# Optimization experiments

Measured on AMD Instinct MI355X. Metric: run time of the kernel, lower is better.

The kernel has to match this reference:

```python
import jax, jax.numpy as jnp
import numpy as np

N_HEADS = 16
D_HEAD = 64
D_MODEL = 1024
WINDOW = 256
B, T = 4, 2048


def rotate_half(x):
    x1, x2 = jnp.split(x, 2, axis=-1)
    return jnp.concatenate([-x2, x1], axis=-1)


def apply_rope(x, cos, sin):
    return x * cos + rotate_half(x) * sin


def setup_inputs() -> dict:
    key = jax.random.key(0)
    ks = jax.random.split(key, 5)
    x = jax.random.normal(ks[0], (B, T, D_MODEL), dtype=jnp.float32)
    cos = jax.random.normal(ks[1], (1, T, 1, D_HEAD), dtype=jnp.float32)
    sin = jax.random.normal(ks[2], (1, T, 1, D_HEAD), dtype=jnp.float32)
    qkv_w = jax.random.normal(ks[3], (3 * D_MODEL, D_MODEL), dtype=jnp.float32) * (D_MODEL ** -0.5)
    out_w = jax.random.normal(ks[4], (D_MODEL, D_MODEL), dtype=jnp.float32) * (D_MODEL ** -0.5)
    return {"x": x, "cos": cos, "sin": sin, "qkv_w": qkv_w, "out_w": out_w}


def reference(x, cos, sin, qkv_w, out_w):
    Bc, Tc, C = x.shape
    # QKV projection (bias-free Linear: y = x @ W^T)
    qkv = jnp.einsum('btc,fc->btf', x, qkv_w)
    q, k, v = jnp.split(qkv, 3, axis=-1)
    # [B, H, T, d]
    def to_heads(t):
        return t.reshape(Bc, Tc, N_HEADS, D_HEAD).transpose(0, 2, 1, 3)
    q, k, v = to_heads(q), to_heads(k), to_heads(v)
    # RoPE: cos/sin [1, T, 1, d] -> [1, 1, T, d] broadcasting over heads
    cos_t = cos[:, :Tc].transpose(0, 2, 1, 3)
    sin_t = sin[:, :Tc].transpose(0, 2, 1, 3)
    q = apply_rope(q, cos_t, sin_t)
    k = apply_rope(k, cos_t, sin_t)
    # banded causal mask: allow j <= i and j >= i - (window-1)
    i = jnp.arange(Tc)[:, None]
    j = jnp.arange(Tc)[None, :]
    allowed = (j <= i) & (j >= i - (WINDOW - 1))  # [T, T]
    scale = 1.0 / jnp.sqrt(jnp.asarray(D_HEAD, dtype=q.dtype))
    scores = jnp.einsum('bhqd,bhkd->bhqk', q, k) * scale
    scores = jnp.where(allowed[None, None], scores, jnp.finfo(scores.dtype).min)
    attn = jax.nn.softmax(scores, axis=-1)
    out = jnp.einsum('bhqk,bhkd->bhqd', attn, v)
    out = out.transpose(0, 2, 1, 3).reshape(Bc, Tc, C)
    return jnp.einsum('btc,oc->bto', out, out_w)
```

## Files before the change

kernel.cpp:

```cpp
#include <hip/hip_runtime.h>

typedef __bf16 bf16_t;
typedef __bf16 bf16x8 __attribute__((ext_vector_type(8)));
typedef __bf16 bf16x4 __attribute__((ext_vector_type(4)));
typedef float f32x4 __attribute__((ext_vector_type(4)));

#define GLOAD_LDS16(gptr, lptr)                                                              \
  __builtin_amdgcn_global_load_lds((const __attribute__((address_space(1))) void*)(gptr),    \
                                   (__attribute__((address_space(3))) void*)(lptr), 16, 0, 0)

__device__ __forceinline__ f32x4 f32x4_zero() {
  f32x4 v; v[0] = 0.f; v[1] = 0.f; v[2] = 0.f; v[3] = 0.f; return v;
}

__global__ void cast3_kernel(const float* __restrict__ a, const float* __restrict__ b,
                             const float* __restrict__ c, bf16_t* __restrict__ oa,
                             bf16_t* __restrict__ ob, bf16_t* __restrict__ oc) {
  int i = blockIdx.x * blockDim.x + threadIdx.x;
  const float* src; bf16_t* dst; int j;
  if (i < 2097152) { src = a; dst = oa; j = i; }
  else if (i < 2883584) { src = b; dst = ob; j = i - 2097152; }
  else { src = c; dst = oc; j = i - 2883584; }
  float4 v = ((const float4*)src)[j];
  bf16x4 o;
  o[0] = (bf16_t)v.x; o[1] = (bf16_t)v.y; o[2] = (bf16_t)v.z; o[3] = (bf16_t)v.w;
  ((bf16x4*)dst)[j] = o;
}

#define GT_AELE 16384
#define GT_BELE 8192
#define GT_TILE (GT_AELE + GT_BELE)

__device__ __forceinline__ void gt_stage(const bf16_t* __restrict__ A,
                                         const bf16_t* __restrict__ B, bf16_t* buf,
                                         int bm, int bn, int t, int K, int tid) {
#pragma unroll
  for (int i = 0; i < 4; i++) {
    int gi = tid + i * 512;
    int row = gi >> 3, g = gi & 7;
    const bf16_t* src = A + (size_t)(bm * 256 + row) * K + t * 64 + ((g ^ (row & 7)) << 3);
    GLOAD_LDS16(src, buf + gi * 8);
  }
#pragma unroll
  for (int i = 0; i < 2; i++) {
    int gi = tid + i * 512;
    int row = gi >> 3, g = gi & 7;
    const bf16_t* src = B + (size_t)(bn * 128 + row) * K + t * 64 + ((g ^ (row & 7)) << 3);
    GLOAD_LDS16(src, buf + GT_AELE + gi * 8);
  }
}

template <int MODE>
__global__ __launch_bounds__(512, 1) void gemm_bt_kernel(
    const bf16_t* __restrict__ A, const bf16_t* __restrict__ B, float* __restrict__ C,
    bf16_t* __restrict__ oq, bf16_t* __restrict__ ok_, bf16_t* __restrict__ ov,
    const float* __restrict__ cosp, const float* __restrict__ sinp,
    int M, int N, int K) {
  __shared__ bf16_t lds[3 * GT_TILE];

  const int tid = threadIdx.x;
  const int lane = tid & 63;
  const int wid = tid >> 6;
  const int wr = wid >> 1;
  const int wc = wid & 1;
  const int l16 = lane & 15;
  const int qd = lane >> 4;
  const int bm = blockIdx.x, bn = blockIdx.y;

  f32x4 acc[4][4];
#pragma unroll
  for (int m = 0; m < 4; m++)
#pragma unroll
    for (int n = 0; n < 4; n++) acc[m][n] = f32x4_zero();

  const int NT = K >> 6;

  gt_stage(A, B, lds, bm, bn, 0, K, tid);
  gt_stage(A, B, lds + GT_TILE, bm, bn, 1, K, tid);
  asm volatile("s_waitcnt vmcnt(6)" ::: "memory");
  __builtin_amdgcn_s_barrier();
  __builtin_amdgcn_sched_barrier(0);

  int s = 0;
  for (int j = 0; j < NT; ++j) {
    if (j + 2 < NT) {
      int s2 = s + 2; if (s2 >= 3) s2 -= 3;
      gt_stage(A, B, lds + s2 * GT_TILE, bm, bn, j + 2, K, tid);
    }

    const bf16_t* bufc = lds + s * GT_TILE;
    bf16x8 af[4][2], bf[4][2];
#pragma unroll
    for (int m = 0; m < 4; m++)
#pragma unroll
      for (int kk = 0; kk < 2; kk++) {
        int row = wr * 64 + m * 16 + l16;
        af[m][kk] = *(const bf16x8*)&bufc[row * 64 + (((kk * 4 + qd) ^ (row & 7)) << 3)];
      }
#pragma unroll
    for (int n = 0; n < 4; n++)
#pragma unroll
      for (int kk = 0; kk < 2; kk++) {
        int row = wc * 64 + n * 16 + l16;
        bf[n][kk] = *(const bf16x8*)&bufc[GT_AELE + row * 64 + (((kk * 4 + qd) ^ (row & 7)) << 3)];
      }

    __builtin_amdgcn_s_setprio(1);
#pragma unroll
    for (int m = 0; m < 4; m++)
#pragma unroll
      for (int n = 0; n < 4; n++)
#pragma unroll
        for (int kk = 0; kk < 2; kk++)
          acc[m][n] = __builtin_amdgcn_mfma_f32_16x16x32_bf16(af[m][kk], bf[n][kk], acc[m][n], 0, 0, 0);
    __builtin_amdgcn_s_setprio(0);

    if (j + 2 < NT) {
      asm volatile("s_waitcnt vmcnt(6)" ::: "memory");
    } else {
      asm volatile("s_waitcnt vmcnt(0)" ::: "memory");
    }
    __builtin_amdgcn_s_barrier();
    __builtin_amdgcn_sched_barrier(0);
    s = (s == 2) ? 0 : s + 1;
  }

  if (MODE == 0) {
#pragma unroll
    for (int m = 0; m < 4; m++)
#pragma unroll
      for (int n = 0; n < 4; n++)
#pragma unroll
        for (int r = 0; r < 4; r++) {
          int row = bm * 256 + wr * 64 + m * 16 + qd * 4 + r;
          int col = bn * 128 + wc * 64 + n * 16 + l16;
          C[(size_t)row * N + col] = acc[m][n][r];
        }
  } else {
    const int colbase = bn * 128 + wc * 64;
    const int part = colbase >> 10;
    const int h = (colbase & 1023) >> 6;
    if (part == 2) {
      bf16_t* lw = lds + wid * 4096;
#pragma unroll
      for (int m = 0; m < 4; m++)
#pragma unroll
        for (int n = 0; n < 4; n++) {
          int d = n * 16 + l16;
          int gr = (m * 2 + (qd >> 1)) ^ (d & 7);
          bf16x4 w;
          w[0] = (bf16_t)acc[m][n][0];
          w[1] = (bf16_t)acc[m][n][1];
          w[2] = (bf16_t)acc[m][n][2];
          w[3] = (bf16_t)acc[m][n][3];
          *(bf16x4*)&lw[d * 64 + gr * 8 + (qd & 1) * 4] = w;
        }
      asm volatile("s_waitcnt lgkmcnt(0)" ::: "memory");
      __builtin_amdgcn_sched_barrier(0);
      const int rowbase = bm * 256 + wr * 64;
      const int bb = rowbase >> 11, tb = rowbase & 2047;
      bf16_t* vbase = ov + ((size_t)(bb * 16 + h) * 64) * 2048 + tb;
#pragma unroll
      for (int it = 0; it < 8; it++) {
        int d = it * 8 + (lane >> 3);
        int g = lane & 7;
        *(bf16x8*)&vbase[(size_t)d * 2048 + g * 8] =
            *(const bf16x8*)&lw[d * 64 + ((g ^ (d & 7)) << 3)];
      }
    } else {
      bf16_t* dst = (part == 0) ? oq : ok_;
      const float qsc = (part == 0) ? 0.18033688011112042f : 1.0f;
#pragma unroll
      for (int m = 0; m < 4; m++)
#pragma unroll
        for (int r = 0; r < 4; r++) {
          int row = bm * 256 + wr * 64 + m * 16 + qd * 4 + r;
          int b = row >> 11, t = row & 2047;
          size_t basei = (((size_t)(b * 16 + h)) * 2048 + t) * 64;
#pragma unroll
          for (int nb = 0; nb < 2; nb++) {
            int d = nb * 16 + l16;
            float xl = acc[m][nb][r];
            float xh = acc[m][nb + 2][r];
            float cl = cosp[t * 64 + d], ch = cosp[t * 64 + d + 32];
            float sl = sinp[t * 64 + d], sh = sinp[t * 64 + d + 32];
            dst[basei + d]      = (bf16_t)((xl * cl - xh * sl) * qsc);
            dst[basei + d + 32] = (bf16_t)((xh * ch + xl * sh) * qsc);
          }
        }
    }
  }
}

__global__ __launch_bounds__(256) void attn_kernel(
    const bf16_t* __restrict__ qh, const bf16_t* __restrict__ kh,
    const bf16_t* __restrict__ vt, bf16_t* __restrict__ ao) {
  __shared__ bf16_t qs[64 * 64];
  __shared__ bf16_t ks[64 * 64];
  __shared__ bf16_t vts[64 * 64];
  __shared__ bf16_t ps[4][16 * 64];

  const int tid = threadIdx.x;
  const int lane = tid & 63;
  const int wid = tid >> 6;
  const int l16 = lane & 15;
  const int qd = lane >> 4;

  const int bh = blockIdx.x;
  const int i0 = blockIdx.y * 64;
  const int b = bh >> 4, h = bh & 15;

  auto swz4 = [](int f) { int r = f >> 3; return r * 8 + ((f & 7) ^ (r & 7)); };

  {
    const uint4* src = (const uint4*)(qh + ((size_t)bh * 2048 + i0) * 64);
    uint4* dst = (uint4*)qs;
    dst[swz4(tid)] = src[tid];
    dst[swz4(tid + 256)] = src[tid + 256];
  }

  bf16x8 bones;
#pragma unroll
  for (int e = 0; e < 8; e++) bones[e] = (bf16_t)1.0f;

  float l_i[4] = {0.f, 0.f, 0.f, 0.f};
  f32x4 oacc[4];
#pragma unroll
  for (int nb = 0; nb < 4; nb++) oacc[nb] = f32x4_zero();

  const int c1 = i0 >> 6;
  const int c0 = (c1 >= 4) ? (c1 - 4) : 0;

  for (int c = c0; c <= c1; c++) {
    const int j0 = c * 64;
    __syncthreads();
    {
      const uint4* ksrc = (const uint4*)(kh + ((size_t)bh * 2048 + j0) * 64);
      uint4* kdst = (uint4*)ks;
      uint4* vdst = (uint4*)vts;
      kdst[swz4(tid)] = ksrc[tid];
      kdst[swz4(tid + 256)] = ksrc[tid + 256];
      {
        int f = tid;
        vdst[swz4(f)] = *(const uint4*)(vt + (size_t)(bh * 64 + (f >> 3)) * 2048 + j0 + (f & 7) * 8);
        f = tid + 256;
        vdst[swz4(f)] = *(const uint4*)(vt + (size_t)(bh * 64 + (f >> 3)) * 2048 + j0 + (f & 7) * 8);
      }
    }
    __syncthreads();

    f32x4 sacc[4];
#pragma unroll
    for (int nb = 0; nb < 4; nb++) sacc[nb] = f32x4_zero();
#pragma unroll
    for (int kk = 0; kk < 2; kk++) {
      bf16x8 afr = *(const bf16x8*)&qs[(wid * 16 + l16) * 64 + (((kk * 4 + qd) ^ (l16 & 7)) * 8)];
#pragma unroll
      for (int nb = 0; nb < 4; nb++) {
        bf16x8 bfr = *(const bf16x8*)&ks[(nb * 16 + l16) * 64 + (((kk * 4 + qd) ^ (l16 & 7)) * 8)];
        sacc[nb] = __builtin_amdgcn_mfma_f32_16x16x32_bf16(afr, bfr, sacc[nb], 0, 0, 0);
      }
    }

#pragma unroll
    for (int r = 0; r < 4; r++) {
      const int i = i0 + wid * 16 + qd * 4 + r;
      const int prow = qd * 4 + r;
#pragma unroll
      for (int nb = 0; nb < 4; nb++) {
        const int j = j0 + nb * 16 + l16;
        bool valid = (j <= i) && (j + 256 > i);
        float p = valid ? exp2f(sacc[nb][r]) : 0.f;
        ps[wid][prow * 64 + (((nb * 2 + (l16 >> 3)) ^ (prow & 7)) * 8) + (l16 & 7)] = (bf16_t)p;
      }
    }

    asm volatile("s_waitcnt lgkmcnt(0)" ::: "memory");
    __builtin_amdgcn_sched_barrier(0);

    f32x4 lacc = f32x4_zero();
#pragma unroll
    for (int kk = 0; kk < 2; kk++) {
      bf16x8 afr = *(const bf16x8*)&ps[wid][l16 * 64 + (((kk * 4 + qd) ^ (l16 & 7)) * 8)];
      lacc = __builtin_amdgcn_mfma_f32_16x16x32_bf16(afr, bones, lacc, 0, 0, 0);
#pragma unroll
      for (int nb = 0; nb < 4; nb++) {
        bf16x8 bfr = *(const bf16x8*)&vts[(nb * 16 + l16) * 64 + (((kk * 4 + qd) ^ (l16 & 7)) * 8)];
        oacc[nb] = __builtin_amdgcn_mfma_f32_16x16x32_bf16(afr, bfr, oacc[nb], 0, 0, 0);
      }
    }
#pragma unroll
    for (int r = 0; r < 4; r++) l_i[r] += lacc[r];
  }

#pragma unroll
  for (int nb = 0; nb < 4; nb++) {
#pragma unroll
    for (int r = 0; r < 4; r++) {
      int t = i0 + wid * 16 + qd * 4 + r;
      ao[((size_t)(b * 2048 + t)) * 1024 + h * 64 + nb * 16 + l16] =
          (bf16_t)(oacc[nb][r] / l_i[r]);
    }
  }
}

extern "C" void kernel_launch(void* const* d_in, const int* in_sizes, int n_in,
                              void* d_out, int out_size, void* d_ws, size_t ws_size,
                              hipStream_t stream) {
  const float* x    = (const float*)d_in[0];
  const float* cosp = (const float*)d_in[1];
  const float* sinp = (const float*)d_in[2];
  const float* qkvw = (const float*)d_in[3];
  const float* outw = (const float*)d_in[4];
  float* out = (float*)d_out;

  char* ws = (char*)d_ws;
  bf16_t* xb  = (bf16_t*)(ws + 0);
  bf16_t* qwb = (bf16_t*)(ws + 16777216);
  bf16_t* owb = (bf16_t*)(ws + 23068672);
  bf16_t* qhp = (bf16_t*)(ws + 25165824);
  bf16_t* khp = (bf16_t*)(ws + 41943040);
  bf16_t* vtp = (bf16_t*)(ws + 58720256);
  bf16_t* aop = (bf16_t*)(ws + 75497472);

  cast3_kernel<<<12288, 256, 0, stream>>>(x, qkvw, outw, xb, qwb, owb);

  gemm_bt_kernel<1><<<dim3(32, 24), 512, 0, stream>>>(xb, qwb, nullptr, qhp, khp, vtp,
                                                      cosp, sinp, 8192, 3072, 1024);
  attn_kernel<<<dim3(64, 32), 256, 0, stream>>>(qhp, khp, vtp, aop);
  gemm_bt_kernel<0><<<dim3(32, 8), 512, 0, stream>>>(aop, owb, out, nullptr, nullptr, nullptr,
                                                     nullptr, nullptr, 8192, 1024, 1024);
}
```

Measured before the change: 214.2 us.

## Process four query tiles per attention block to reuse K/V tiles

Each attention block now covers 256 query rows as four 64-row tiles held in shared memory, instead of a single 64-row tile. It walks the K/V tiles of the combined band once and applies each loaded tile to every query tile whose window includes it. This cuts redundant global K/V loads, since each tile was previously fetched by up to five blocks. In exchange the grid shrinks fourfold, shared-memory and accumulator register use grow, and the per-block loop becomes longer and more serial. The K/V buffers are indexed by iteration parity, but both barriers remain, so loads do not actually overlap with compute.

```diff
diff --git a/kernel.cpp b/kernel.cpp
--- a/kernel.cpp
+++ b/kernel.cpp
@@ -195,9 +195,9 @@
 __global__ __launch_bounds__(256) void attn_kernel(
     const bf16_t* __restrict__ qh, const bf16_t* __restrict__ kh,
     const bf16_t* __restrict__ vt, bf16_t* __restrict__ ao) {
-  __shared__ bf16_t qs[64 * 64];
-  __shared__ bf16_t ks[64 * 64];
-  __shared__ bf16_t vts[64 * 64];
+  __shared__ bf16_t qs[4][64 * 64];
+  __shared__ bf16_t ks[2][64 * 64];
+  __shared__ bf16_t vts[2][64 * 64];
   __shared__ bf16_t ps[4][16 * 64];
 
   const int tid = threadIdx.x;
@@ -207,101 +207,116 @@
   const int qd = lane >> 4;
 
   const int bh = blockIdx.x;
-  const int i0 = blockIdx.y * 64;
+  const int chunk = blockIdx.y;
   const int b = bh >> 4, h = bh & 15;
 
   auto swz4 = [](int f) { int r = f >> 3; return r * 8 + ((f & 7) ^ (r & 7)); };
 
   {
-    const uint4* src = (const uint4*)(qh + ((size_t)bh * 2048 + i0) * 64);
-    uint4* dst = (uint4*)qs;
-    dst[swz4(tid)] = src[tid];
-    dst[swz4(tid + 256)] = src[tid + 256];
+    const uint4* src = (const uint4*)(qh + ((size_t)bh * 2048 + chunk * 256) * 64);
+#pragma unroll
+    for (int qt = 0; qt < 4; qt++) {
+      uint4* dst = (uint4*)qs[qt];
+      dst[swz4(tid)] = src[qt * 512 + tid];
+      dst[swz4(tid + 256)] = src[qt * 512 + tid + 256];
+    }
   }
 
   bf16x8 bones;
 #pragma unroll
   for (int e = 0; e < 8; e++) bones[e] = (bf16_t)1.0f;
 
-  float l_i[4] = {0.f, 0.f, 0.f, 0.f};
-  f32x4 oacc[4];
-#pragma unroll
-  for (int nb = 0; nb < 4; nb++) oacc[nb] = f32x4_zero();
-
-  const int c1 = i0 >> 6;
-  const int c0 = (c1 >= 4) ? (c1 - 4) : 0;
+  f32x4 oacc[4][4];
+  float l_i[4][4];
+#pragma unroll
+  for (int qt = 0; qt < 4; qt++)
+#pragma unroll
+    for (int nb = 0; nb < 4; nb++) {
+      oacc[qt][nb] = f32x4_zero();
+      l_i[qt][nb] = 0.f;
+    }
+
+  const int cbase = chunk * 4;
+  const int c0 = (cbase >= 4) ? cbase - 4 : 0;
+  const int c1 = cbase + 3;
 
   for (int c = c0; c <= c1; c++) {
-    const int j0 = c * 64;
+    const int p = c & 1;
     __syncthreads();
     {
-      const uint4* ksrc = (const uint4*)(kh + ((size_t)bh * 2048 + j0) * 64);
-      uint4* kdst = (uint4*)ks;
-      uint4* vdst = (uint4*)vts;
+      const uint4* ksrc = (const uint4*)(kh + ((size_t)bh * 2048 + c * 64) * 64);
+      uint4* kdst = (uint4*)ks[p];
+      uint4* vdst = (uint4*)vts[p];
       kdst[swz4(tid)] = ksrc[tid];
       kdst[swz4(tid + 256)] = ksrc[tid + 256];
-      {
-        int f = tid;
-        vdst[swz4(f)] = *(const uint4*)(vt + (size_t)(bh * 64 + (f >> 3)) * 2048 + j0 + (f & 7) * 8);
-        f = tid + 256;
-        vdst[swz4(f)] = *(const uint4*)(vt + (size_t)(bh * 64 + (f >> 3)) * 2048 + j0 + (f & 7) * 8);
-      }
+      int f = tid;
+      vdst[swz4(f)] = *(const uint4*)(vt + (size_t)(bh * 64 + (f >> 3)) * 2048 + c * 64 + (f & 7) * 8);
+      f = tid + 256;
+      vdst[swz4(f)] = *(const uint4*)(vt + (size_t)(bh * 64 + (f >> 3)) * 2048 + c * 64 + (f & 7) * 8);
     }
     __syncthreads();
 
-    f32x4 sacc[4];
-#pragma unroll
-    for (int nb = 0; nb < 4; nb++) sacc[nb] = f32x4_zero();
-#pragma unroll
-    for (int kk = 0; kk < 2; kk++) {
-      bf16x8 afr = *(const bf16x8*)&qs[(wid * 16 + l16) * 64 + (((kk * 4 + qd) ^ (l16 & 7)) * 8)];
-#pragma unroll
-      for (int nb = 0; nb < 4; nb++) {
-        bf16x8 bfr = *(const bf16x8*)&ks[(nb * 16 + l16) * 64 + (((kk * 4 + qd) ^ (l16 & 7)) * 8)];
-        sacc[nb] = __builtin_amdgcn_mfma_f32_16x16x32_bf16(afr, bfr, sacc[nb], 0, 0, 0);
-      }
-    }
-
-#pragma unroll
-    for (int r = 0; r < 4; r++) {
-      const int i = i0 + wid * 16 + qd * 4 + r;
-      const int prow = qd * 4 + r;
-#pragma unroll
-      for (int nb = 0; nb < 4; nb++) {
-        const int j = j0 + nb * 16 + l16;
-        bool valid = (j <= i) && (j + 256 > i);
-        float p = valid ? exp2f(sacc[nb][r]) : 0.f;
-        ps[wid][prow * 64 + (((nb * 2 + (l16 >> 3)) ^ (prow & 7)) * 8) + (l16 & 7)] = (bf16_t)p;
-      }
-    }
-
-    asm volatile("s_waitcnt lgkmcnt(0)" ::: "memory");
-    __builtin_amdgcn_sched_barrier(0);
-
-    f32x4 lacc = f32x4_zero();
-#pragma unroll
-    for (int kk = 0; kk < 2; kk++) {
-      bf16x8 afr = *(const bf16x8*)&ps[wid][l16 * 64 + (((kk * 4 + qd) ^ (l16 & 7)) * 8)];
-      lacc = __builtin_amdgcn_mfma_f32_16x16x32_bf16(afr, bones, lacc, 0, 0, 0);
-#pragma unroll
-      for (int nb = 0; nb < 4; nb++) {
-        bf16x8 bfr = *(const bf16x8*)&vts[(nb * 16 + l16) * 64 + (((kk * 4 + qd) ^ (l16 & 7)) * 8)];
-        oacc[nb] = __builtin_amdgcn_mfma_f32_16x16x32_bf16(afr, bfr, oacc[nb], 0, 0, 0);
-      }
-    }
-#pragma unroll
-    for (int r = 0; r < 4; r++) l_i[r] += lacc[r];
-  }
-
-#pragma unroll
-  for (int nb = 0; nb < 4; nb++) {
-#pragma unroll
-    for (int r = 0; r < 4; r++) {
-      int t = i0 + wid * 16 + qd * 4 + r;
-      ao[((size_t)(b * 2048 + t)) * 1024 + h * 64 + nb * 16 + l16] =
-          (bf16_t)(oacc[nb][r] / l_i[r]);
-    }
-  }
+    const int lc = c - cbase;
+#pragma unroll
+    for (int qt = 0; qt < 4; qt++) {
+      if (qt < lc || qt > lc + 4) continue;
+      const int i0q = chunk * 256 + qt * 64;
+
+      f32x4 sacc[4];
+#pragma unroll
+      for (int nb = 0; nb < 4; nb++) sacc[nb] = f32x4_zero();
+#pragma unroll
+      for (int kk = 0; kk < 2; kk++) {
+        bf16x8 afr = *(const bf16x8*)&qs[qt][(wid * 16 + l16) * 64 + (((kk * 4 + qd) ^ (l16 & 7)) * 8)];
+#pragma unroll
+        for (int nb = 0; nb < 4; nb++) {
+          bf16x8 bfr = *(const bf16x8*)&ks[p][(nb * 16 + l16) * 64 + (((kk * 4 + qd) ^ (l16 & 7)) * 8)];
+          sacc[nb] = __builtin_amdgcn_mfma_f32_16x16x32_bf16(afr, bfr, sacc[nb], 0, 0, 0);
+        }
+      }
+
+#pragma unroll
+      for (int r = 0; r < 4; r++) {
+        const int i = i0q + wid * 16 + qd * 4 + r;
+        const int prow = qd * 4 + r;
+#pragma unroll
+        for (int nb = 0; nb < 4; nb++) {
+          const int j = c * 64 + nb * 16 + l16;
+          bool valid = (j <= i) && (j + 256 > i);
+          float pv = valid ? exp2f(sacc[nb][r]) : 0.f;
+          ps[wid][prow * 64 + (((nb * 2 + (l16 >> 3)) ^ (prow & 7)) * 8) + (l16 & 7)] = (bf16_t)pv;
+        }
+      }
+
+      asm volatile("s_waitcnt lgkmcnt(0)" ::: "memory");
+      __builtin_amdgcn_sched_barrier(0);
+
+      f32x4 lacc = f32x4_zero();
+#pragma unroll
+      for (int kk = 0; kk < 2; kk++) {
+        bf16x8 afr = *(const bf16x8*)&ps[wid][l16 * 64 + (((kk * 4 + qd) ^ (l16 & 7)) * 8)];
+        lacc = __builtin_amdgcn_mfma_f32_16x16x32_bf16(afr, bones, lacc, 0, 0, 0);
+#pragma unroll
+        for (int nb = 0; nb < 4; nb++) {
+          bf16x8 bfr = *(const bf16x8*)&vts[p][(nb * 16 + l16) * 64 + (((kk * 4 + qd) ^ (l16 & 7)) * 8)];
+          oacc[qt][nb] = __builtin_amdgcn_mfma_f32_16x16x32_bf16(afr, bfr, oacc[qt][nb], 0, 0, 0);
+        }
+      }
+#pragma unroll
+      for (int r = 0; r < 4; r++) l_i[qt][r] += lacc[r];
+    }
+  }
+
+#pragma unroll
+  for (int qt = 0; qt < 4; qt++)
+#pragma unroll
+    for (int nb = 0; nb < 4; nb++)
+#pragma unroll
+      for (int r = 0; r < 4; r++) {
+        int t = chunk * 256 + qt * 64 + wid * 16 + qd * 4 + r;
+        ao[((size_t)(b * 2048 + t)) * 1024 + h * 64 + nb * 16 + l16] =
+            (bf16_t)(oacc[qt][nb][r] / l_i[qt][r]);
+      }
 }
 
 extern "C" void kernel_launch(void* const* d_in, const int* in_sizes, int n_in,
@@ -327,7 +342,7 @@
 
   gemm_bt_kernel<1><<<dim3(32, 24), 512, 0, stream>>>(xb, qwb, nullptr, qhp, khp, vtp,
                                                       cosp, sinp, 8192, 3072, 1024);
-  attn_kernel<<<dim3(64, 32), 256, 0, stream>>>(qhp, khp, vtp, aop);
+  attn_kernel<<<dim3(64, 8), 256, 0, stream>>>(qhp, khp, vtp, aop);
   gemm_bt_kernel<0><<<dim3(32, 8), 512, 0, stream>>>(aop, owb, out, nullptr, nullptr, nullptr,
                                                      nullptr, nullptr, 8192, 1024, 1024);
 }
```

Result: faster. 209.6 us (-2.2%).
